# Optimization experiments

Measured on AMD Instinct MI355X. Metric: run time of the kernel, lower is better.

The kernel has to match this reference:

```python
import jax, jax.numpy as jnp
import numpy as np
from jax import lax

# dims: B batch, C=d_model=256, IMG=128, P=4 patch, H=W=32, L=H*W=1024
# D=d_inner=512 (ssm_ratio 2.0), N=d_state=16, R=dt_rank=16, K=4 scan directions
B, C, IMG, P = 2, 256, 128, 4
H = W = IMG // P
L = H * W
D_INNER, N, R, K = 512, 16, 16, 4


def layernorm(x, g, b, eps=1e-5):
    mu = jnp.mean(x, axis=-1, keepdims=True)
    var = jnp.var(x, axis=-1, keepdims=True)
    return (x - mu) * lax.rsqrt(var + eps) * g + b


def setup_inputs() -> dict:
    key = jax.random.key(0)
    ks = jax.random.split(key, 12)
    f = lambda i, shape, s=0.02: jax.random.normal(ks[i], shape, jnp.float32) * s
    A_init = jnp.tile(jnp.arange(1, N + 1, dtype=jnp.float32)[None, None, :], (K, D_INNER, 1))
    return {
        "x": jax.random.normal(ks[0], (B, C, IMG, IMG), jnp.float32),
        "patch_w": f(1, (C, C, P, P)),
        "patch_b": jnp.zeros((C,), jnp.float32),
        "ln_g": jnp.ones((C,), jnp.float32),
        "ln_b": jnp.zeros((C,), jnp.float32),
        "in_w": f(2, (2 * D_INNER, C)),
        "conv_w": f(3, (D_INNER, 1, 3, 3)),
        "conv_b": jnp.zeros((D_INNER,), jnp.float32),
        "xproj_w": f(4, (K, R + 2 * N, D_INNER)),
        "dt_w": f(5, (K, D_INNER, R)),
        "dt_b": f(6, (K, D_INNER), 0.1),
        "A_log": jnp.log(A_init),
        "Ds": jnp.ones((K, D_INNER), jnp.float32),
        "on_g": jnp.ones((D_INNER,), jnp.float32),
        "on_b": jnp.zeros((D_INNER,), jnp.float32),
        "out_w": f(7, (C, D_INNER)),
        "head_w": f(8, (1, C)),
        "head_b": jnp.zeros((1,), jnp.float32),
    }


def _forward(x, patch_w, patch_b, ln_g, ln_b, in_w, conv_w, conv_b, xproj_w,
             dt_w, dt_b, A_log, Ds, on_g, on_b, out_w, head_w, head_b):
    dn = ("NCHW", "OIHW", "NCHW")
    # GRL is identity in forward. Patch embed conv, stride = patch.
    t = lax.conv_general_dilated(x, patch_w, (P, P), "VALID", dimension_numbers=dn)
    t = t + patch_b[None, :, None, None]
    t = jnp.transpose(t, (0, 2, 3, 1))                      # (B,H,W,C)

    # ---- VSS block: t + SS2D(LN(t)) ----
    u = layernorm(t, ln_g, ln_b)
    xz = jnp.einsum("bhwc,ec->bhwe", u, in_w)               # (B,H,W,2D)
    xc, z = jnp.split(xz, 2, axis=-1)
    xc = jnp.transpose(xc, (0, 3, 1, 2))                    # (B,D,H,W)
    xc = lax.conv_general_dilated(xc, conv_w, (1, 1), "SAME",
                                  dimension_numbers=dn, feature_group_count=D_INNER)
    xc = jax.nn.silu(xc + conv_b[None, :, None, None])

    # cross-scan: row-major, col-major, and their reverses -> (B,K,D,L)
    x_hw = xc.reshape(B, D_INNER, L)
    x_wh = jnp.transpose(xc, (0, 1, 3, 2)).reshape(B, D_INNER, L)
    xs = jnp.stack([x_hw, x_wh], axis=1)
    xs = jnp.concatenate([xs, jnp.flip(xs, axis=-1)], axis=1)  # (B,4,D,L)

    x_dbl = jnp.einsum("bkdl,kcd->bkcl", xs, xproj_w)          # (B,K,R+2N,L)
    dts_r = x_dbl[:, :, :R]
    Bs = x_dbl[:, :, R:R + N]                                  # (B,K,N,L)
    Cs = x_dbl[:, :, R + N:]                                   # (B,K,N,L)
    dts = jnp.einsum("bkrl,kdr->bkdl", dts_r, dt_w) + dt_b[None, :, :, None]
    dts = jax.nn.softplus(dts)                                 # (B,K,D,L)

    A = -jnp.exp(A_log)                                        # (K,D,N)
    dA = jnp.exp(dts[:, :, :, None, :] * A[None, :, :, :, None])      # (B,K,D,N,L)
    dBu = (dts * xs)[:, :, :, None, :] * Bs[:, :, None, :, :]         # (B,K,D,N,L)

    dA_t = jnp.moveaxis(dA, -1, 0)        # (L,B,K,D,N)
    dBu_t = jnp.moveaxis(dBu, -1, 0)
    Cs_t = jnp.moveaxis(Cs, -1, 0)        # (L,B,K,N)

    def step(h, inputs):
        dA_i, dBu_i, C_i = inputs
        h = dA_i * h + dBu_i
        y = jnp.einsum("bkdn,bkn->bkd", h, C_i)
        return h, y

    h0 = jnp.zeros((B, K, D_INNER, N), xs.dtype)
    _, ys = lax.scan(step, h0, (dA_t, dBu_t, Cs_t))           # ys: (L,B,K,D)
    ys = jnp.moveaxis(ys, 0, -1)                               # (B,K,D,L)
    ys = ys + Ds[None, :, :, None] * xs

    # cross-merge (invert the 4 scan orders and sum)
    y_rev = jnp.flip(ys[:, 2:], axis=-1)                        # (B,2,D,L)
    y_hw = ys[:, 0] + y_rev[:, 0]
    y_wh = ys[:, 1] + y_rev[:, 1]
    y_wh = jnp.transpose(y_wh.reshape(B, D_INNER, W, H), (0, 1, 3, 2)).reshape(B, D_INNER, L)
    y = (y_hw + y_wh).reshape(B, D_INNER, H, W)
    y = jnp.transpose(y, (0, 2, 3, 1))                          # (B,H,W,D)

    y = layernorm(y, on_g, on_b) * jax.nn.silu(z)
    ss_out = jnp.einsum("bhwd,cd->bhwc", y, out_w)
    t = t + ss_out

    # global average pool + head
    pooled = jnp.mean(t, axis=(1, 2))                           # (B,C)
    return pooled @ head_w.T + head_b


def reference(x, patch_w, patch_b, ln_g, ln_b, in_w, conv_w, conv_b, xproj_w,
              dt_w, dt_b, A_log, Ds, on_g, on_b, out_w, head_w, head_b):
    return _forward(x, patch_w, patch_b, ln_g, ln_b, in_w, conv_w, conv_b, xproj_w,
                    dt_w, dt_b, A_log, Ds, on_g, on_b, out_w, head_w, head_b)
```

## Files before the change

### kernel.cpp

```cpp
#include <hip/hip_runtime.h>
#include <math.h>


typedef __attribute__((ext_vector_type(4))) float f32x4;
typedef __attribute__((ext_vector_type(8))) short bf16x8;

__device__ __forceinline__ ushort bf16_rn(float f) {
  uint u = __float_as_uint(f);
  return (ushort)((u + 0x7fffu + ((u >> 16) & 1u)) >> 16);
}
__device__ __forceinline__ float bf2f(uint us) { return __uint_as_float(us << 16); }
__device__ __forceinline__ uint packbf(float a, float b) {
  return (uint)bf16_rn(a) | ((uint)bf16_rn(b) << 16);
}

__global__ __launch_bounds__(256) void split_all(
    const float* __restrict__ pw, const float* __restrict__ iw,
    const float* __restrict__ ow, const float* __restrict__ xw,
    ushort* __restrict__ pwh, ushort* __restrict__ pwl,
    ushort* __restrict__ iwh, ushort* __restrict__ iwl,
    ushort* __restrict__ owh, ushort* __restrict__ owl,
    ushort* __restrict__ xwh, ushort* __restrict__ xwl) {
  int i = blockIdx.x * 256 + threadIdx.x;
  const float* src; ushort* hi; ushort* lo; int off;
  if (i < 1048576)      { src = pw; hi = pwh; lo = pwl; off = i; }
  else if (i < 1310720) { src = iw; hi = iwh; lo = iwl; off = i - 1048576; }
  else if (i < 1441792) { src = ow; hi = owh; lo = owl; off = i - 1310720; }
  else if (i < 1540096) { src = xw; hi = xwh; lo = xwl; off = i - 1441792; }
  else return;
  float f = src[off];
  ushort h = bf16_rn(f);
  hi[off] = h;
  lo[off] = bf16_rn(f - __uint_as_float(((uint)h) << 16));
}

__global__ __launch_bounds__(256) void im2col_bf16(const float* __restrict__ x,
    ushort* __restrict__ Ap) {
  __shared__ __align__(16) ushort tile[32][136];
  int c0 = blockIdx.x * 8, hh = blockIdx.y, b = blockIdx.z;
  int tid = threadIdx.x;
  int ci = tid >> 5, ph = (tid >> 3) & 3, w4 = tid & 7;
  const float* src = x + (((long)(b * 256 + c0 + ci) * 128 + 4 * hh + ph) * 128 + 16 * w4);
  #pragma unroll
  for (int j = 0; j < 4; ++j) {
    float4 v = *(const float4*)(src + 4 * j);
    uint2 pk;
    pk.x = packbf(v.x, v.y);
    pk.y = packbf(v.z, v.w);
    *(uint2*)&tile[w4 * 4 + j][ci * 16 + ph * 4] = pk;
  }
  __syncthreads();
  int w = tid >> 3;
  long rowbase = ((long)(b * 1024 + hh * 32 + w)) * 4096 + c0 * 16;
  #pragma unroll
  for (int i = 0; i < 2; ++i) {
    int gr = (tid & 7) + 8 * i;
    *(uint4*)&Ap[rowbase + gr * 8] = *(const uint4*)&tile[w][gr * 8];
  }
}

__global__ __launch_bounds__(512) void mfma_bf(
    const ushort* __restrict__ A, const ushort* __restrict__ Bhi,
    const ushort* __restrict__ Blo, float* __restrict__ Cout, float* __restrict__ C2,
    int M, int N, int K, int kchunk, int mode)
{
  __shared__ __align__(16) ushort Ah[128 * 64];
  __shared__ __align__(16) ushort Bh[64 * 64];
  __shared__ __align__(16) ushort Bl[64 * 64];
  int tid = threadIdx.x;
  int n0 = blockIdx.x * 64;
  int m0 = blockIdx.y * 128;
  int k0 = blockIdx.z * kchunk;
  int wid = tid >> 6, lane = tid & 63;
  int wm = wid >> 1, wn = wid & 1;
  int lrow = lane & 15, g = lane >> 4;
  f32x4 acc[2][2] = {};
  int nkt = kchunk >> 6;
  for (int kt = 0; kt < nkt; ++kt) {
    int kb = k0 + (kt << 6);
    {
      int gi = tid & 7;
      #pragma unroll
      for (int i = 0; i < 2; ++i) {
        int row = (tid >> 3) + (i << 6);
        uint4 v = *(const uint4*)&A[(long)(m0 + row) * K + kb + gi * 8];
        *(uint4*)&Ah[row * 64 + ((gi ^ (row & 7)) << 3)] = v;
      }
      int row = tid >> 3;
      long off = (long)(n0 + row) * K + kb + gi * 8;
      int la = row * 64 + ((gi ^ (row & 7)) << 3);
      *(uint4*)&Bh[la] = *(const uint4*)&Bhi[off];
      *(uint4*)&Bl[la] = *(const uint4*)&Blo[off];
    }
    __syncthreads();
    #pragma unroll
    for (int kk = 0; kk < 2; ++kk) {
      bf16x8 af[2], bhf[2], blf[2];
      #pragma unroll
      for (int mi = 0; mi < 2; ++mi) {
        int row = wm * 32 + mi * 16 + lrow;
        af[mi] = *(const bf16x8*)&Ah[row * 64 + ((((kk << 2) + g) ^ (row & 7)) << 3)];
      }
      #pragma unroll
      for (int ni = 0; ni < 2; ++ni) {
        int row = wn * 32 + ni * 16 + lrow;
        int col = (((kk << 2) + g) ^ (row & 7)) << 3;
        bhf[ni] = *(const bf16x8*)&Bh[row * 64 + col];
        blf[ni] = *(const bf16x8*)&Bl[row * 64 + col];
      }
      #pragma unroll
      for (int mi = 0; mi < 2; ++mi)
        #pragma unroll
        for (int ni = 0; ni < 2; ++ni) {
          acc[mi][ni] = __builtin_amdgcn_mfma_f32_16x16x32_bf16(af[mi], bhf[ni], acc[mi][ni], 0, 0, 0);
          acc[mi][ni] = __builtin_amdgcn_mfma_f32_16x16x32_bf16(af[mi], blf[ni], acc[mi][ni], 0, 0, 0);
        }
    }
    __syncthreads();
  }
  int r4 = lane >> 4;
  if (mode == 2) {
    bool xhalf = (n0 < 512);
    ushort* xcb = (ushort*)Cout;
    #pragma unroll
    for (int mi = 0; mi < 2; ++mi)
      #pragma unroll
      for (int ni = 0; ni < 2; ++ni) {
        int n = n0 + wn * 32 + ni * 16 + lrow;
        int mb = m0 + wm * 32 + mi * 16 + r4 * 4;
        int bb = mb >> 10, l = mb & 1023;
        if (xhalf) {
          uint2 o;
          o.x = packbf(acc[mi][ni][0], acc[mi][ni][1]);
          o.y = packbf(acc[mi][ni][2], acc[mi][ni][3]);
          *(uint2*)&xcb[((long)(bb * 512 + n)) * 1024 + l] = o;
        } else {
          #pragma unroll
          for (int r = 0; r < 4; ++r)
            C2[(long)(mb + r) * 512 + (n - 512)] = acc[mi][ni][r];
        }
      }
  } else {
    long zoff = (long)blockIdx.z * M * N;
    #pragma unroll
    for (int mi = 0; mi < 2; ++mi)
      #pragma unroll
      for (int ni = 0; ni < 2; ++ni) {
        int n = n0 + wn * 32 + ni * 16 + lrow;
        int mb = m0 + wm * 32 + mi * 16 + r4 * 4;
        #pragma unroll
        for (int r = 0; r < 4; ++r)
          Cout[zoff + (long)(mb + r) * N + n] = acc[mi][ni][r];
      }
  }
}

__global__ __launch_bounds__(256) void mfma_x(
    const ushort* __restrict__ A, const ushort* __restrict__ Bhi,
    const ushort* __restrict__ Blo, float* __restrict__ xdbl)
{
  __shared__ __align__(16) ushort Ah[64 * 64];
  __shared__ __align__(16) ushort Bh[48 * 64];
  __shared__ __align__(16) ushort Bl[48 * 64];
  int tid = threadIdx.x;
  int m0 = blockIdx.x * 64;
  int z = blockIdx.y, k = z & 3;
  const ushort* Az = A + (long)z * 524288;
  const ushort* Bhz = Bhi + (long)k * 24576;
  const ushort* Blz = Blo + (long)k * 24576;
  int lane = tid & 63, wv = tid >> 6;
  int lrow = lane & 15, g = lane >> 4;
  f32x4 acc[3] = {};
  for (int kt = 0; kt < 8; ++kt) {
    int kb = kt << 6;
    #pragma unroll
    for (int i = 0; i < 2; ++i) {
      int idx = i * 256 + tid;
      int row = idx >> 3, gi = idx & 7;
      uint4 v = *(const uint4*)&Az[(long)(m0 + row) * 512 + kb + gi * 8];
      *(uint4*)&Ah[row * 64 + ((gi ^ (row & 7)) << 3)] = v;
      if (idx < 384) {
        long off = (long)row * 512 + kb + gi * 8;
        int la = row * 64 + ((gi ^ (row & 7)) << 3);
        *(uint4*)&Bh[la] = *(const uint4*)&Bhz[off];
        *(uint4*)&Bl[la] = *(const uint4*)&Blz[off];
      }
    }
    __syncthreads();
    #pragma unroll
    for (int kk = 0; kk < 2; ++kk) {
      int arow = wv * 16 + lrow;
      bf16x8 af = *(const bf16x8*)&Ah[arow * 64 + ((((kk << 2) + g) ^ (arow & 7)) << 3)];
      #pragma unroll
      for (int ni = 0; ni < 3; ++ni) {
        int brow = ni * 16 + lrow;
        int col = (((kk << 2) + g) ^ (brow & 7)) << 3;
        bf16x8 bh = *(const bf16x8*)&Bh[brow * 64 + col];
        bf16x8 bl = *(const bf16x8*)&Bl[brow * 64 + col];
        acc[ni] = __builtin_amdgcn_mfma_f32_16x16x32_bf16(af, bh, acc[ni], 0, 0, 0);
        acc[ni] = __builtin_amdgcn_mfma_f32_16x16x32_bf16(af, bl, acc[ni], 0, 0, 0);
      }
    }
    __syncthreads();
  }
  float* Cz = xdbl + (long)z * 49152;
  int r4 = lane >> 4;
  #pragma unroll
  for (int ni = 0; ni < 3; ++ni) {
    int n = ni * 16 + lrow;
    int mb = m0 + wv * 16 + r4 * 4;
    #pragma unroll
    for (int r = 0; r < 4; ++r)
      Cz[(long)(mb + r) * 48 + n] = acc[ni][r];
  }
}

__global__ __launch_bounds__(256) void reduce_split(const float* __restrict__ P,
    float* __restrict__ C, const float* __restrict__ bias,
    int MN, int N, int S, int accumulate) {
  int i = blockIdx.x * 256 + threadIdx.x;
  if (i * 4 >= MN) return;
  float4 v = make_float4(0.f, 0.f, 0.f, 0.f);
  for (int s = 0; s < S; ++s) {
    float4 p = *(const float4*)(P + (long)s * MN + i * 4);
    v.x += p.x; v.y += p.y; v.z += p.z; v.w += p.w;
  }
  if (bias) {
    float4 bv = *(const float4*)(bias + ((i * 4) & (N - 1)));
    v.x += bv.x; v.y += bv.y; v.z += bv.z; v.w += bv.w;
  }
  if (accumulate) {
    float4 o = *(const float4*)(C + (long)i * 4);
    v.x += o.x; v.y += o.y; v.z += o.z; v.w += o.w;
  }
  *(float4*)(C + (long)i * 4) = v;
}

__device__ __forceinline__ float blk_sum(float v, float* sm) {
  #pragma unroll
  for (int o = 32; o > 0; o >>= 1) v += __shfl_down(v, o);
  int wid = threadIdx.x >> 6, lane = threadIdx.x & 63;
  __syncthreads();
  if (lane == 0) sm[wid] = v;
  __syncthreads();
  int nw = blockDim.x >> 6;
  float r = 0.f;
  for (int i = 0; i < nw; ++i) r += sm[i];
  return r;
}

__global__ __launch_bounds__(256) void reduce_ln1(const float* __restrict__ P,
    float* __restrict__ t, const float* __restrict__ bias,
    const float* __restrict__ g, const float* __restrict__ b,
    ushort* __restrict__ u) {
  __shared__ float sm[8];
  int m = blockIdx.x, c = threadIdx.x;
  float v = bias[c];
  #pragma unroll
  for (int s = 0; s < 8; ++s) v += P[(long)s * 524288 + m * 256 + c];
  t[(long)m * 256 + c] = v;
  float s1 = blk_sum(v, sm);
  float s2 = blk_sum(v * v, sm);
  float mu = s1 * (1.f / 256.f);
  float var = s2 * (1.f / 256.f) - mu * mu;
  float rs = rsqrtf(var + 1e-5f);
  u[(long)m * 256 + c] = bf16_rn((v - mu) * rs * g[c] + b[c]);
}

__global__ __launch_bounds__(256) void dwconv_kernel(const ushort* __restrict__ xc,
    const float* __restrict__ cw, const float* __restrict__ cb, ushort* __restrict__ out) {
  __shared__ float plane[32][33];
  int d = blockIdx.x, b = blockIdx.y;
  long base = ((long)b * 512 + d) * 1024;
  int tid = threadIdx.x;
  uint2 v = *(const uint2*)&xc[base + tid * 4];
  int h0 = (tid * 4) >> 5, w0 = (tid * 4) & 31;
  plane[h0][w0 + 0] = bf2f(v.x & 0xffff); plane[h0][w0 + 1] = bf2f(v.x >> 16);
  plane[h0][w0 + 2] = bf2f(v.y & 0xffff); plane[h0][w0 + 3] = bf2f(v.y >> 16);
  float w9[9];
  #pragma unroll
  for (int i = 0; i < 9; ++i) w9[i] = cw[d * 9 + i];
  float bias = cb[d];
  __syncthreads();
  float o4[4];
  #pragma unroll
  for (int j = 0; j < 4; ++j) {
    int p = tid * 4 + j, h = p >> 5, w = p & 31;
    float acc = 0.f;
    #pragma unroll
    for (int dh = -1; dh <= 1; ++dh) {
      int hy = h + dh;
      if (hy < 0 || hy > 31) continue;
      #pragma unroll
      for (int dw = -1; dw <= 1; ++dw) {
        int wx = w + dw;
        if (wx < 0 || wx > 31) continue;
        acc += w9[(dh + 1) * 3 + (dw + 1)] * plane[hy][wx];
      }
    }
    acc += bias;
    o4[j] = acc / (1.f + __expf(-acc));
  }
  uint2 o2;
  o2.x = packbf(o4[0], o4[1]);
  o2.y = packbf(o4[2], o4[3]);
  *(uint2*)&out[base + tid * 4] = o2;
}

__global__ __launch_bounds__(256) void build_xsT(const ushort* __restrict__ xca,
    ushort* __restrict__ xsTb) {
  __shared__ ushort tile[32][34];
  int h = blockIdx.x;
  int d0 = blockIdx.y * 32;
  int z = blockIdx.z;
  int b = z >> 2, k = z & 3;
  int tid = threadIdx.x;
  int a = tid >> 5, q = tid & 31;
  #pragma unroll
  for (int i = 0; i < 4; ++i) {
    int di = a + i * 8;
    tile[di][q] = xca[((long)(b * 512 + d0 + di)) * 1024 + h * 32 + q];
  }
  __syncthreads();
  #pragma unroll
  for (int i = 0; i < 4; ++i) {
    int w = a + i * 8;
    int r;
    if (k == 0) r = h * 32 + w;
    else if (k == 1) r = w * 32 + h;
    else if (k == 2) r = 1023 - (h * 32 + w);
    else r = 1023 - (w * 32 + h);
    xsTb[((long)z * 1024 + r) * 512 + d0 + q] = tile[q][w];
  }
}

template<bool FINAL>
__global__ __launch_bounds__(128) void scan_chunk6(
    const float* __restrict__ xdbl, ushort* xsb,
    const float* __restrict__ dtw, const float* __restrict__ dtb,
    const float* __restrict__ A_log, const float* __restrict__ Ds,
    float* __restrict__ Pb, float* __restrict__ hpb)
{
  __shared__ float sdt[32][64];
  __shared__ float sxv[16][64];
  __shared__ float sy[16][64];
  __shared__ float sBC[32][32];
  float (*sR)[16] = (float(*)[16])sy;
  int tid = threadIdx.x;
  int dl = tid >> 1, ng = tid & 1;
  int d0 = blockIdx.x * 64;
  int d = d0 + dl;
  int c = blockIdx.y;
  int z = blockIdx.z;
  int k = z & 3;
  long baseD = (long)z * 524288;
  int l0 = c * 32;
  const float* xdz = xdbl + (long)z * 49152 + (long)l0 * 48;
  #pragma unroll
  for (int i = 0; i < 2; ++i) {
    int idx = i * 128 + tid;
    int l = idx >> 3, q = idx & 7;
    *(float4*)&sBC[l][q * 4] = *(const float4*)(xdz + l * 48 + 16 + q * 4);
  }
  {
    int l = tid >> 2, q = tid & 3;
    *(float4*)&sR[l][q * 4] = *(const float4*)(xdz + l * 48 + q * 4);
  }
  float a[8], h[8];
  #pragma unroll
  for (int j = 0; j < 8; ++j) {
    a[j] = -__expf(A_log[((long)k * 512 + d) * 16 + ng * 8 + j]);
    h[j] = 0.f;
  }
  float4 wr0 = *(const float4*)(dtw + ((long)k * 512 + d) * 16);
  float4 wr1 = *(const float4*)(dtw + ((long)k * 512 + d) * 16 + 4);
  float4 wr2 = *(const float4*)(dtw + ((long)k * 512 + d) * 16 + 8);
  float4 wr3 = *(const float4*)(dtw + ((long)k * 512 + d) * 16 + 12);
  float dbias = dtb[k * 512 + d];
  int gbase = c * 65536 + z * 8192 + d * 16 + ng * 8;
  float Dv = 0.f;
  if (FINAL) {
    #pragma unroll
    for (int j = 0; j < 8; ++j) h[j] = hpb[gbase + j];
    Dv = Ds[k * 512 + d];
  }
  __syncthreads();
  #pragma unroll
  for (int li = 0; li < 16; ++li) {
    int l = ng * 16 + li;
    const float* rr = &sR[l][0];
    float acc = dbias;
    acc += wr0.x * rr[0];  acc += wr0.y * rr[1];  acc += wr0.z * rr[2];  acc += wr0.w * rr[3];
    acc += wr1.x * rr[4];  acc += wr1.y * rr[5];  acc += wr1.z * rr[6];  acc += wr1.w * rr[7];
    acc += wr2.x * rr[8];  acc += wr2.y * rr[9];  acc += wr2.z * rr[10]; acc += wr2.w * rr[11];
    acc += wr3.x * rr[12]; acc += wr3.y * rr[13]; acc += wr3.z * rr[14]; acc += wr3.w * rr[15];
    sdt[l][dl] = (acc > 20.f) ? acc : __logf(1.f + __expf(acc));
  }
  __syncthreads();
  int xli = tid >> 3;
  int xdj = (tid & 7) * 8;
  uint4 rxv = *(const uint4*)&xsb[baseD + (long)(l0 + xli) * 512 + d0 + xdj];
  float dtsum = 0.f;
  for (int t = 0; t < 2; ++t) {
    {
      float4 f0, f1;
      f0.x = bf2f(rxv.x & 0xffff); f0.y = bf2f(rxv.x >> 16);
      f0.z = bf2f(rxv.y & 0xffff); f0.w = bf2f(rxv.y >> 16);
      f1.x = bf2f(rxv.z & 0xffff); f1.y = bf2f(rxv.z >> 16);
      f1.z = bf2f(rxv.w & 0xffff); f1.w = bf2f(rxv.w >> 16);
      *(float4*)&sxv[xli][xdj] = f0;
      *(float4*)&sxv[xli][xdj + 4] = f1;
    }
    __syncthreads();
    if (t == 0)
      rxv = *(const uint4*)&xsb[baseD + (long)(l0 + 16 + xli) * 512 + d0 + xdj];
    #pragma unroll
    for (int li = 0; li < 16; ++li) {
      int lr = t * 16 + li;
      float dt = sdt[lr][dl];
      float xv = sxv[li][dl];
      float w = dt * xv;
      float4 B0 = *(const float4*)&sBC[lr][ng * 8];
      float4 B1 = *(const float4*)&sBC[lr][ng * 8 + 4];
      if (!FINAL) {
        dtsum += dt;
        h[0] = __expf(dt * a[0]) * h[0] + w * B0.x;
        h[1] = __expf(dt * a[1]) * h[1] + w * B0.y;
        h[2] = __expf(dt * a[2]) * h[2] + w * B0.z;
        h[3] = __expf(dt * a[3]) * h[3] + w * B0.w;
        h[4] = __expf(dt * a[4]) * h[4] + w * B1.x;
        h[5] = __expf(dt * a[5]) * h[5] + w * B1.y;
        h[6] = __expf(dt * a[6]) * h[6] + w * B1.z;
        h[7] = __expf(dt * a[7]) * h[7] + w * B1.w;
      } else {
        float4 C0 = *(const float4*)&sBC[lr][16 + ng * 8];
        float4 C1 = *(const float4*)&sBC[lr][16 + ng * 8 + 4];
        float p;
        h[0] = __expf(dt * a[0]) * h[0] + w * B0.x; p  = h[0] * C0.x;
        h[1] = __expf(dt * a[1]) * h[1] + w * B0.y; p += h[1] * C0.y;
        h[2] = __expf(dt * a[2]) * h[2] + w * B0.z; p += h[2] * C0.z;
        h[3] = __expf(dt * a[3]) * h[3] + w * B0.w; p += h[3] * C0.w;
        h[4] = __expf(dt * a[4]) * h[4] + w * B1.x; p += h[4] * C1.x;
        h[5] = __expf(dt * a[5]) * h[5] + w * B1.y; p += h[5] * C1.y;
        h[6] = __expf(dt * a[6]) * h[6] + w * B1.z; p += h[6] * C1.z;
        h[7] = __expf(dt * a[7]) * h[7] + w * B1.w; p += h[7] * C1.w;
        p += __shfl_xor(p, 1);
        if (ng == 0) sy[li][dl] = p + Dv * xv;
      }
    }
    __syncthreads();
    if (FINAL) {
      float4 f0 = *(float4*)&sy[xli][xdj];
      float4 f1 = *(float4*)&sy[xli][xdj + 4];
      uint4 o;
      o.x = packbf(f0.x, f0.y); o.y = packbf(f0.z, f0.w);
      o.z = packbf(f1.x, f1.y); o.w = packbf(f1.z, f1.w);
      *(uint4*)&xsb[baseD + (long)(l0 + t * 16 + xli) * 512 + d0 + xdj] = o;
    }
  }
  if (!FINAL) {
    float4 pv;
    #pragma unroll
    for (int i = 0; i < 2; ++i) {
      pv.x = __expf(dtsum * a[i * 4 + 0]);
      pv.y = __expf(dtsum * a[i * 4 + 1]);
      pv.z = __expf(dtsum * a[i * 4 + 2]);
      pv.w = __expf(dtsum * a[i * 4 + 3]);
      *(float4*)(Pb + gbase + i * 4) = pv;
      *(float4*)(hpb + gbase + i * 4) = make_float4(h[i*4+0], h[i*4+1], h[i*4+2], h[i*4+3]);
    }
  }
}

__global__ __launch_bounds__(256) void scan_prefix(const float* __restrict__ Pb,
    float* __restrict__ hpb) {
  int g = blockIdx.x * 256 + threadIdx.x;
  float h = 0.f;
  #pragma unroll
  for (int c = 0; c < 32; ++c) {
    float P = Pb[c * 65536 + g];
    float hp = hpb[c * 65536 + g];
    hpb[c * 65536 + g] = h;
    h = P * h + hp;
  }
}

__global__ __launch_bounds__(256) void combine_ln2gate(const ushort* __restrict__ ys,
    const float* __restrict__ zb, ushort* __restrict__ out,
    const float* __restrict__ g, const float* __restrict__ b) {
  __shared__ float sm[8];
  int m = blockIdx.x, tid = threadIdx.x;
  int bb = m >> 10, l = m & 1023;
  int hh = l >> 5, w = l & 31;
  int lw = w * 32 + hh;
  long b4 = (long)bb * 4;
  uint u0 = *(const uint*)&ys[((b4 + 0) * 1024 + l) * 512 + tid * 2];
  uint u1 = *(const uint*)&ys[((b4 + 2) * 1024 + (1023 - l)) * 512 + tid * 2];
  uint u2 = *(const uint*)&ys[((b4 + 1) * 1024 + lw) * 512 + tid * 2];
  uint u3 = *(const uint*)&ys[((b4 + 3) * 1024 + (1023 - lw)) * 512 + tid * 2];
  float v0 = bf2f(u0 & 0xffff) + bf2f(u1 & 0xffff) + bf2f(u2 & 0xffff) + bf2f(u3 & 0xffff);
  float v1 = bf2f(u0 >> 16) + bf2f(u1 >> 16) + bf2f(u2 >> 16) + bf2f(u3 >> 16);
  float s1 = blk_sum(v0 + v1, sm);
  float s2 = blk_sum(v0 * v0 + v1 * v1, sm);
  float mu = s1 * (1.f / 512.f);
  float var = s2 * (1.f / 512.f) - mu * mu;
  float rs = rsqrtf(var + 1e-5f);
  float2 gg = *(const float2*)(g + tid * 2);
  float2 bbv = *(const float2*)(b + tid * 2);
  float2 zz = *(const float2*)(zb + (long)m * 512 + tid * 2);
  float y0 = ((v0 - mu) * rs * gg.x + bbv.x) * (zz.x / (1.f + __expf(-zz.x)));
  float y1 = ((v1 - mu) * rs * gg.y + bbv.y) * (zz.y / (1.f + __expf(-zz.y)));
  *(uint*)&out[(long)m * 512 + tid * 2] = packbf(y0, y1);
}

__global__ __launch_bounds__(256) void head_partial(const float* __restrict__ t,
    const float* __restrict__ hw, float* __restrict__ part) {
  __shared__ float sm[8];
  int j = blockIdx.x, b = blockIdx.y;
  int c = threadIdx.x;
  float s = 0.f;
  for (int l = j * 64; l < j * 64 + 64; ++l) s += t[((long)b * 1024 + l) * 256 + c];
  s *= hw[c];
  float tot = blk_sum(s, sm);
  if (c == 0) part[b * 16 + j] = tot;
}

__global__ void head_final(const float* __restrict__ part, const float* __restrict__ hb, float* __restrict__ out) {
  int tid = threadIdx.x;
  float v = (tid < 32) ? part[tid] : 0.f;
  #pragma unroll
  for (int o = 1; o < 16; o <<= 1) v += __shfl_xor(v, o);
  if (tid < 32 && (tid & 15) == 0) out[tid >> 4] = v * (1.f / 1024.f) + hb[0];
}

extern "C" void kernel_launch(void* const* d_in, const int* in_sizes, int n_in,
                              void* d_out, int out_size, void* d_ws, size_t ws_size,
                              hipStream_t stream) {
  const float* x       = (const float*)d_in[0];
  const float* patch_w = (const float*)d_in[1];
  const float* patch_b = (const float*)d_in[2];
  const float* ln_g    = (const float*)d_in[3];
  const float* ln_b    = (const float*)d_in[4];
  const float* in_w    = (const float*)d_in[5];
  const float* conv_w  = (const float*)d_in[6];
  const float* conv_b  = (const float*)d_in[7];
  const float* xproj_w = (const float*)d_in[8];
  const float* dt_w    = (const float*)d_in[9];
  const float* dt_b    = (const float*)d_in[10];
  const float* A_log   = (const float*)d_in[11];
  const float* Ds      = (const float*)d_in[12];
  const float* on_g    = (const float*)d_in[13];
  const float* on_b    = (const float*)d_in[14];
  const float* out_w   = (const float*)d_in[15];
  const float* head_w  = (const float*)d_in[16];
  const float* head_b  = (const float*)d_in[17];

  float* ws = (float*)d_ws;
  float* t_buf   = ws;
  float* u_buf   = t_buf + 524288;
  float* xz_buf  = u_buf + 524288;
  float* xc_buf  = xz_buf + 2097152;
  float* xca_buf = xc_buf + 1048576;
  float* xsT_buf = xca_buf + 1048576;
  float* xdbl_buf= xsT_buf + 4194304;
  float* spl_buf = xdbl_buf + 393216;
  float* part_buf= spl_buf + 4194304;
  float* tail    = part_buf + 32;
  ushort* A_p    = (ushort*)xsT_buf;
  ushort* pw_hi  = (ushort*)xz_buf;
  ushort* pw_lo  = (ushort*)(xz_buf + 524288);
  float*  z_buf  = xz_buf;
  float*  P_patch= spl_buf;
  float*  P_out  = spl_buf;
  ushort* u_bf   = (ushort*)u_buf;
  ushort* xc_bf  = (ushort*)xc_buf;
  ushort* xca_bf = (ushort*)xca_buf;
  ushort* y_bf   = (ushort*)xca_buf;
  ushort* iw_hi  = (ushort*)tail;
  ushort* iw_lo  = (ushort*)(tail + 131072);
  ushort* ow_hi  = (ushort*)(tail + 262144);
  ushort* ow_lo  = (ushort*)(tail + 327680);
  ushort* xw_hi  = (ushort*)(tail + 393216);
  ushort* xw_lo  = (ushort*)(tail + 442368);
  ushort* xsT_bf = (ushort*)(tail + 491520);
  float*  P_buf  = tail + 2588672;
  float*  hp_buf = tail + 4685824;

  split_all<<<6017, 256, 0, stream>>>(patch_w, in_w, out_w, xproj_w,
      pw_hi, pw_lo, iw_hi, iw_lo, ow_hi, ow_lo, xw_hi, xw_lo);
  im2col_bf16<<<dim3(32, 32, 2), 256, 0, stream>>>(x, A_p);
  mfma_bf<<<dim3(4, 16, 8), 512, 0, stream>>>(A_p, pw_hi, pw_lo, P_patch, nullptr,
      2048, 256, 4096, 512, 0);
  reduce_ln1<<<2048, 256, 0, stream>>>(P_patch, t_buf, patch_b, ln_g, ln_b, u_bf);
  mfma_bf<<<dim3(16, 16, 1), 512, 0, stream>>>(u_bf, iw_hi, iw_lo, xc_buf, z_buf,
      2048, 1024, 256, 256, 2);
  dwconv_kernel<<<dim3(512, 2), 256, 0, stream>>>(xc_bf, conv_w, conv_b, xca_bf);
  build_xsT<<<dim3(32, 16, 8), 256, 0, stream>>>(xca_bf, xsT_bf);
  mfma_x<<<dim3(16, 8), 256, 0, stream>>>(xsT_bf, xw_hi, xw_lo, xdbl_buf);
  scan_chunk6<false><<<dim3(8, 32, 8), 128, 0, stream>>>(xdbl_buf, xsT_bf,
      dt_w, dt_b, A_log, Ds, P_buf, hp_buf);
  scan_prefix<<<256, 256, 0, stream>>>(P_buf, hp_buf);
  scan_chunk6<true><<<dim3(8, 32, 8), 128, 0, stream>>>(xdbl_buf, xsT_bf,
      dt_w, dt_b, A_log, Ds, nullptr, hp_buf);
  combine_ln2gate<<<2048, 256, 0, stream>>>(xsT_bf, z_buf, y_bf, on_g, on_b);
  mfma_bf<<<dim3(4, 16, 4), 512, 0, stream>>>(y_bf, ow_hi, ow_lo, P_out, nullptr,
      2048, 256, 512, 128, 0);
  reduce_split<<<512, 256, 0, stream>>>(P_out, t_buf, nullptr, 524288, 256, 4, 1);
  head_partial<<<dim3(16, 2), 256, 0, stream>>>(t_buf, head_w, part_buf);
  head_final<<<1, 64, 0, stream>>>(part_buf, head_b, (float*)d_out);
}
```

Before: 140.8 us.

## Merge prep kernels, linearize GEMM block order, store chunk dt sums instead of decays

Fuses the weight hi/lo split and im2col into one prep kernel, which removes a launch. The GEMM grid is flattened to 1D, with the K-split index varying fastest so that blocks sharing the same A/B tiles run close together, which should help L2 reuse. The chunked scan now writes one dt sum per (chunk, direction, channel) instead of 16 decay factors per state, and the prefix kernel recomputes exp(dtsum*A) itself, which cuts memory traffic. In exchange the prefix kernel does extra exp work and reads A_log.

```diff
diff --git a/kernel.cpp b/kernel.cpp
--- a/kernel.cpp
+++ b/kernel.cpp
@@ -14,63 +14,66 @@
   return (uint)bf16_rn(a) | ((uint)bf16_rn(b) << 16);
 }
 
-__global__ __launch_bounds__(256) void split_all(
+__global__ __launch_bounds__(256) void prep_kernel(const float* __restrict__ x,
+    ushort* __restrict__ Ap,
     const float* __restrict__ pw, const float* __restrict__ iw,
     const float* __restrict__ ow, const float* __restrict__ xw,
     ushort* __restrict__ pwh, ushort* __restrict__ pwl,
     ushort* __restrict__ iwh, ushort* __restrict__ iwl,
     ushort* __restrict__ owh, ushort* __restrict__ owl,
     ushort* __restrict__ xwh, ushort* __restrict__ xwl) {
-  int i = blockIdx.x * 256 + threadIdx.x;
-  const float* src; ushort* hi; ushort* lo; int off;
-  if (i < 1048576)      { src = pw; hi = pwh; lo = pwl; off = i; }
-  else if (i < 1310720) { src = iw; hi = iwh; lo = iwl; off = i - 1048576; }
-  else if (i < 1441792) { src = ow; hi = owh; lo = owl; off = i - 1310720; }
-  else if (i < 1540096) { src = xw; hi = xwh; lo = xwl; off = i - 1441792; }
-  else return;
-  float f = src[off];
-  ushort h = bf16_rn(f);
-  hi[off] = h;
-  lo[off] = bf16_rn(f - __uint_as_float(((uint)h) << 16));
-}
-
-__global__ __launch_bounds__(256) void im2col_bf16(const float* __restrict__ x,
-    ushort* __restrict__ Ap) {
-  __shared__ __align__(16) ushort tile[32][136];
-  int c0 = blockIdx.x * 8, hh = blockIdx.y, b = blockIdx.z;
+  int bid = blockIdx.x;
   int tid = threadIdx.x;
-  int ci = tid >> 5, ph = (tid >> 3) & 3, w4 = tid & 7;
-  const float* src = x + (((long)(b * 256 + c0 + ci) * 128 + 4 * hh + ph) * 128 + 16 * w4);
-  #pragma unroll
-  for (int j = 0; j < 4; ++j) {
-    float4 v = *(const float4*)(src + 4 * j);
-    uint2 pk;
-    pk.x = packbf(v.x, v.y);
-    pk.y = packbf(v.z, v.w);
-    *(uint2*)&tile[w4 * 4 + j][ci * 16 + ph * 4] = pk;
-  }
-  __syncthreads();
-  int w = tid >> 3;
-  long rowbase = ((long)(b * 1024 + hh * 32 + w)) * 4096 + c0 * 16;
-  #pragma unroll
-  for (int i = 0; i < 2; ++i) {
-    int gr = (tid & 7) + 8 * i;
-    *(uint4*)&Ap[rowbase + gr * 8] = *(const uint4*)&tile[w][gr * 8];
+  if (bid < 2048) {
+    __shared__ __align__(16) ushort tile[32][136];
+    int b = bid >> 10, hh = (bid >> 5) & 31, c0 = (bid & 31) * 8;
+    int ci = tid >> 5, ph = (tid >> 3) & 3, w4 = tid & 7;
+    const float* src = x + (((long)(b * 256 + c0 + ci) * 128 + 4 * hh + ph) * 128 + 16 * w4);
+    #pragma unroll
+    for (int j = 0; j < 4; ++j) {
+      float4 v = *(const float4*)(src + 4 * j);
+      uint2 pk;
+      pk.x = packbf(v.x, v.y);
+      pk.y = packbf(v.z, v.w);
+      *(uint2*)&tile[w4 * 4 + j][ci * 16 + ph * 4] = pk;
+    }
+    __syncthreads();
+    int w = tid >> 3;
+    long rowbase = ((long)(b * 1024 + hh * 32 + w)) * 4096 + c0 * 16;
+    #pragma unroll
+    for (int i = 0; i < 2; ++i) {
+      int gr = (tid & 7) + 8 * i;
+      *(uint4*)&Ap[rowbase + gr * 8] = *(const uint4*)&tile[w][gr * 8];
+    }
+  } else {
+    int i = (bid - 2048) * 256 + tid;
+    const float* src; ushort* hi; ushort* lo; int off;
+    if (i < 1048576)      { src = pw; hi = pwh; lo = pwl; off = i; }
+    else if (i < 1310720) { src = iw; hi = iwh; lo = iwl; off = i - 1048576; }
+    else if (i < 1441792) { src = ow; hi = owh; lo = owl; off = i - 1310720; }
+    else if (i < 1540096) { src = xw; hi = xwh; lo = xwl; off = i - 1441792; }
+    else return;
+    float f = src[off];
+    ushort h = bf16_rn(f);
+    hi[off] = h;
+    lo[off] = bf16_rn(f - __uint_as_float(((uint)h) << 16));
   }
 }
 
 __global__ __launch_bounds__(512) void mfma_bf(
     const ushort* __restrict__ A, const ushort* __restrict__ Bhi,
     const ushort* __restrict__ Blo, float* __restrict__ Cout, float* __restrict__ C2,
-    int M, int N, int K, int kchunk, int mode)
+    int M, int N, int K, int kchunk, int mode, int NBM, int NBZ)
 {
   __shared__ __align__(16) ushort Ah[128 * 64];
   __shared__ __align__(16) ushort Bh[64 * 64];
   __shared__ __align__(16) ushort Bl[64 * 64];
   int tid = threadIdx.x;
-  int n0 = blockIdx.x * 64;
-  int m0 = blockIdx.y * 128;
-  int k0 = blockIdx.z * kchunk;
+  int bid = blockIdx.x;
+  int kz = bid % NBZ;
+  int n0 = (bid / (NBZ * NBM)) * 64;
+  int m0 = ((bid / NBZ) % NBM) * 128;
+  int k0 = kz * kchunk;
   int wid = tid >> 6, lane = tid & 63;
   int wm = wid >> 1, wn = wid & 1;
   int lrow = lane & 15, g = lane >> 4;
@@ -141,7 +144,7 @@
         }
       }
   } else {
-    long zoff = (long)blockIdx.z * M * N;
+    long zoff = (long)kz * M * N;
     #pragma unroll
     for (int mi = 0; mi < 2; ++mi)
       #pragma unroll
@@ -339,7 +342,7 @@
     const float* __restrict__ xdbl, ushort* xsb,
     const float* __restrict__ dtw, const float* __restrict__ dtb,
     const float* __restrict__ A_log, const float* __restrict__ Ds,
-    float* __restrict__ Pb, float* __restrict__ hpb)
+    float* __restrict__ dsum, float* __restrict__ hpb)
 {
   __shared__ float sdt[32][64];
   __shared__ float sxv[16][64];
@@ -459,26 +462,23 @@
     }
   }
   if (!FINAL) {
-    float4 pv;
-    #pragma unroll
-    for (int i = 0; i < 2; ++i) {
-      pv.x = __expf(dtsum * a[i * 4 + 0]);
-      pv.y = __expf(dtsum * a[i * 4 + 1]);
-      pv.z = __expf(dtsum * a[i * 4 + 2]);
-      pv.w = __expf(dtsum * a[i * 4 + 3]);
-      *(float4*)(Pb + gbase + i * 4) = pv;
-      *(float4*)(hpb + gbase + i * 4) = make_float4(h[i*4+0], h[i*4+1], h[i*4+2], h[i*4+3]);
-    }
-  }
-}
-
-__global__ __launch_bounds__(256) void scan_prefix(const float* __restrict__ Pb,
-    float* __restrict__ hpb) {
+    *(float4*)(hpb + gbase)     = make_float4(h[0], h[1], h[2], h[3]);
+    *(float4*)(hpb + gbase + 4) = make_float4(h[4], h[5], h[6], h[7]);
+    if (ng == 0) dsum[c * 4096 + z * 512 + d] = dtsum;
+  }
+}
+
+__global__ __launch_bounds__(256) void scan_prefix(const float* __restrict__ dsum,
+    const float* __restrict__ A_log, float* __restrict__ hpb) {
   int g = blockIdx.x * 256 + threadIdx.x;
+  int z = g >> 13, n = g & 15;
+  int d = (g >> 4) & 511;
+  int k = z & 3;
+  float a = -__expf(A_log[((long)k * 512 + d) * 16 + n]);
   float h = 0.f;
   #pragma unroll
   for (int c = 0; c < 32; ++c) {
-    float P = Pb[c * 65536 + g];
+    float P = __expf(dsum[c * 4096 + z * 512 + d] * a);
     float hp = hpb[c * 65536 + g];
     hpb[c * 65536 + g] = h;
     h = P * h + hp;
@@ -583,28 +583,27 @@
   ushort* xw_hi  = (ushort*)(tail + 393216);
   ushort* xw_lo  = (ushort*)(tail + 442368);
   ushort* xsT_bf = (ushort*)(tail + 491520);
-  float*  P_buf  = tail + 2588672;
-  float*  hp_buf = tail + 4685824;
-
-  split_all<<<6017, 256, 0, stream>>>(patch_w, in_w, out_w, xproj_w,
+  float*  dsum_buf = tail + 2588672;
+  float*  hp_buf   = tail + 2719744;
+
+  prep_kernel<<<8065, 256, 0, stream>>>(x, A_p, patch_w, in_w, out_w, xproj_w,
       pw_hi, pw_lo, iw_hi, iw_lo, ow_hi, ow_lo, xw_hi, xw_lo);
-  im2col_bf16<<<dim3(32, 32, 2), 256, 0, stream>>>(x, A_p);
-  mfma_bf<<<dim3(4, 16, 8), 512, 0, stream>>>(A_p, pw_hi, pw_lo, P_patch, nullptr,
-      2048, 256, 4096, 512, 0);
+  mfma_bf<<<512, 512, 0, stream>>>(A_p, pw_hi, pw_lo, P_patch, nullptr,
+      2048, 256, 4096, 512, 0, 16, 8);
   reduce_ln1<<<2048, 256, 0, stream>>>(P_patch, t_buf, patch_b, ln_g, ln_b, u_bf);
-  mfma_bf<<<dim3(16, 16, 1), 512, 0, stream>>>(u_bf, iw_hi, iw_lo, xc_buf, z_buf,
-      2048, 1024, 256, 256, 2);
+  mfma_bf<<<256, 512, 0, stream>>>(u_bf, iw_hi, iw_lo, xc_buf, z_buf,
+      2048, 1024, 256, 256, 2, 16, 1);
   dwconv_kernel<<<dim3(512, 2), 256, 0, stream>>>(xc_bf, conv_w, conv_b, xca_bf);
   build_xsT<<<dim3(32, 16, 8), 256, 0, stream>>>(xca_bf, xsT_bf);
   mfma_x<<<dim3(16, 8), 256, 0, stream>>>(xsT_bf, xw_hi, xw_lo, xdbl_buf);
   scan_chunk6<false><<<dim3(8, 32, 8), 128, 0, stream>>>(xdbl_buf, xsT_bf,
-      dt_w, dt_b, A_log, Ds, P_buf, hp_buf);
-  scan_prefix<<<256, 256, 0, stream>>>(P_buf, hp_buf);
+      dt_w, dt_b, A_log, Ds, dsum_buf, hp_buf);
+  scan_prefix<<<256, 256, 0, stream>>>(dsum_buf, A_log, hp_buf);
   scan_chunk6<true><<<dim3(8, 32, 8), 128, 0, stream>>>(xdbl_buf, xsT_bf,
       dt_w, dt_b, A_log, Ds, nullptr, hp_buf);
   combine_ln2gate<<<2048, 256, 0, stream>>>(xsT_bf, z_buf, y_bf, on_g, on_b);
-  mfma_bf<<<dim3(4, 16, 4), 512, 0, stream>>>(y_bf, ow_hi, ow_lo, P_out, nullptr,
-      2048, 256, 512, 128, 0);
+  mfma_bf<<<256, 512, 0, stream>>>(y_bf, ow_hi, ow_lo, P_out, nullptr,
+      2048, 256, 512, 128, 0, 16, 4);
   reduce_split<<<512, 256, 0, stream>>>(P_out, t_buf, nullptr, 524288, 256, 4, 1);
   head_partial<<<dim3(16, 2), 256, 0, stream>>>(t_buf, head_w, part_buf);
   head_final<<<1, 64, 0, stream>>>(part_buf, head_b, (float*)d_out);
```

Result: faster. 133.3 us (-5.3%).
